# Kernel optimization log

Measured on AMD Instinct MI355X. Metric: run time of the kernel, lower is better.

## Reference

```python
import jax, jax.numpy as jnp
import numpy as np

B, C, H, W = 4, 256, 48, 48
NH = 4                 # num_heads
HD = C // NH           # head_dim = 64
KD = HD // 2           # key_dim = 32 (attn_ratio=0.5)
QKV_C = C + 2 * KD * NH  # 512
FF = 2 * C             # 512
EPS = 1e-3             # ultralytics BatchNorm2d eps


def _bn(x, g, b, m, v):
    # eval-mode BatchNorm2d over channel dim 1 of NCHW
    s = g / jnp.sqrt(v + EPS)
    return x * s[:, None, None] + (b - m * s)[:, None, None]


def _conv1x1(x, w):
    # w: [out_c, in_c]
    return jnp.einsum('bchw,oc->bohw', x, w)


def _dwconv3x3(x, w):
    # depthwise 3x3, padding 1; w: [C, 1, 3, 3]
    return jax.lax.conv_general_dilated(
        x, w, (1, 1), [(1, 1), (1, 1)],
        dimension_numbers=('NCHW', 'OIHW', 'NCHW'),
        feature_group_count=C)


def setup_inputs() -> dict:
    key = jax.random.key(0)
    ks = jax.random.split(key, 32)
    d = {}
    d['x'] = jax.random.normal(ks[0], (B, C, H, W), dtype=jnp.float32)

    def bn_params(i, ch):
        g = 0.5 + jax.random.uniform(ks[i], (ch,), dtype=jnp.float32)
        b = 0.1 * jax.random.normal(ks[i + 1], (ch,), dtype=jnp.float32)
        m = 0.1 * jax.random.normal(ks[i + 2], (ch,), dtype=jnp.float32)
        v = 0.5 + jax.random.uniform(ks[i + 3], (ch,), dtype=jnp.float32)
        return g, b, m, v

    d['qkv_w'] = 0.05 * jax.random.normal(ks[1], (QKV_C, C), dtype=jnp.float32)
    d['qkv_g'], d['qkv_b'], d['qkv_m'], d['qkv_v'] = bn_params(2, QKV_C)
    d['pe_w'] = 0.1 * jax.random.normal(ks[6], (C, 1, 3, 3), dtype=jnp.float32)
    d['pe_g'], d['pe_b'], d['pe_m'], d['pe_v'] = bn_params(7, C)
    d['proj_w'] = 0.05 * jax.random.normal(ks[11], (C, C), dtype=jnp.float32)
    d['proj_g'], d['proj_b'], d['proj_m'], d['proj_v'] = bn_params(12, C)
    d['f1_w'] = 0.05 * jax.random.normal(ks[16], (FF, C), dtype=jnp.float32)
    d['f1_g'], d['f1_b'], d['f1_m'], d['f1_v'] = bn_params(17, FF)
    d['f2_w'] = 0.05 * jax.random.normal(ks[21], (C, FF), dtype=jnp.float32)
    d['f2_g'], d['f2_b'], d['f2_m'], d['f2_v'] = bn_params(22, C)
    return d


def reference(x, qkv_w, qkv_g, qkv_b, qkv_m, qkv_v,
              pe_w, pe_g, pe_b, pe_m, pe_v,
              proj_w, proj_g, proj_b, proj_m, proj_v,
              f1_w, f1_g, f1_b, f1_m, f1_v,
              f2_w, f2_g, f2_b, f2_m, f2_v):
    b, c, h, w = x.shape
    n = h * w
    # --- Attention ---
    qkv = _bn(_conv1x1(x, qkv_w), qkv_g, qkv_b, qkv_m, qkv_v)
    qkv = qkv.reshape(b, NH, 2 * KD + HD, n)
    q = qkv[:, :, :KD]            # [b, nh, kd, n]
    k = qkv[:, :, KD:2 * KD]      # [b, nh, kd, n]
    v = qkv[:, :, 2 * KD:]        # [b, nh, hd, n]
    attn = jnp.einsum('bhkn,bhkm->bhnm', q, k) * (KD ** -0.5)
    attn = jax.nn.softmax(attn, axis=-1)
    o = jnp.einsum('bhdm,bhnm->bhdn', v, attn).reshape(b, c, h, w)
    pe = _bn(_dwconv3x3(v.reshape(b, c, h, w), pe_w), pe_g, pe_b, pe_m, pe_v)
    attn_out = _bn(_conv1x1(o + pe, proj_w), proj_g, proj_b, proj_m, proj_v)
    x = x + attn_out  # shortcut
    # --- FFN ---
    f = _conv1x1(x, f1_w)
    f = _bn(f, f1_g, f1_b, f1_m, f1_v)
    f = f * jax.nn.sigmoid(f)  # SiLU
    f = _bn(_conv1x1(f, f2_w), f2_g, f2_b, f2_m, f2_v)
    return x + f  # shortcut
```

## Files before the change

### kernel.cpp

```cpp
#include <hip/hip_runtime.h>
#include <math.h>

#define Bb   4
#define Cc   256
#define Hh   48
#define Ww   48
#define NNp  2304
#define Rr   9216
#define NHd  4
#define QKVC 512
#define EPSf 1e-3f

typedef unsigned int   u32;
typedef unsigned short u16;
typedef __attribute__((ext_vector_type(8))) __bf16 bf16x8;
typedef __attribute__((ext_vector_type(4))) float  f32x4;

#if __has_builtin(__builtin_amdgcn_exp2f)
#define EXP2F(x) __builtin_amdgcn_exp2f(x)
#else
#define EXP2F(x) __expf((x) * 0.6931471805599453f)
#endif

__device__ __forceinline__ u16 f2bf(float f) {
    u32 u = __float_as_uint(f);
    u = (u + 0x7fffu + ((u >> 16) & 1u)) >> 16;
    return (u16)u;
}
__device__ __forceinline__ float bf2f(u16 h) {
    return __uint_as_float((u32)h << 16);
}
__device__ __forceinline__ u32 pk2bf(float a, float b) {
    union { __bf16 h; u16 u; } ua, ub;
    ua.h = (__bf16)a; ub.h = (__bf16)b;
    return (u32)ua.u | ((u32)ub.u << 16);
}
__device__ __forceinline__ void gload16(const void* gsrc, void* ldst) {
    __builtin_amdgcn_global_load_lds(
        (const __attribute__((address_space(1))) u32*)gsrc,
        (__attribute__((address_space(3))) u32*)ldst, 16, 0, 0);
}

__global__ __launch_bounds__(64)
void prep_w(const float* __restrict__ W, const float* __restrict__ g,
            const float* __restrict__ b, const float* __restrict__ m,
            const float* __restrict__ v, u16* __restrict__ Wb,
            float* __restrict__ bias, int K, int qmode)
{
    const int oc = blockIdx.x;
    const int lane = threadIdx.x;
    const float s = g[oc] * rsqrtf(v[oc] + EPSf);
    const float c = (qmode == 1 && (oc & 127) < 32)
                  ? (0.17677669529663687f * 1.4426950408889634f) : 1.f;
    if (lane == 0) bias[oc] = (b[oc] - m[oc] * s) * c;
    const float sc = s * c;
    for (int k0 = lane * 4; k0 < K; k0 += 256) {
        const float4 w = *(const float4*)(W + (size_t)oc * K + k0);
        u32 lo = (u32)f2bf(w.x * sc) | ((u32)f2bf(w.y * sc) << 16);
        u32 hi = (u32)f2bf(w.z * sc) | ((u32)f2bf(w.w * sc) << 16);
        *(uint2*)(Wb + (size_t)oc * K + k0) = make_uint2(lo, hi);
    }
}

__global__ __launch_bounds__(256)
void cvt_x(const float* __restrict__ x, u16* __restrict__ Xt)
{
    const int b = blockIdx.z, c0 = blockIdx.y * 64, n0 = blockIdx.x * 64;
    __shared__ float tile[64][65];
    const int tid = threadIdx.x;
    {
        const int n = tid & 63, cl = tid >> 6;
        #pragma unroll
        for (int cc = 0; cc < 16; ++cc) {
            const int c = cc * 4 + cl;
            tile[c][n] = x[((size_t)b * Cc + c0 + c) * NNp + n0 + n];
        }
    }
    __syncthreads();
    {
        const int n = tid >> 2, q = tid & 3;
        #pragma unroll
        for (int j = 0; j < 2; ++j) {
            const int ch = q * 2 + j, c = ch * 8;
            u32 w[4];
            #pragma unroll
            for (int e = 0; e < 4; ++e)
                w[e] = (u32)f2bf(tile[c + 2*e][n]) | ((u32)f2bf(tile[c + 2*e + 1][n]) << 16);
            *(uint4*)(Xt + ((size_t)b * NNp + n0 + n) * Cc + c0 + c)
                = make_uint4(w[0], w[1], w[2], w[3]);
        }
    }
}

template<int BN_, int FN_, int MODE>
__global__ __launch_bounds__(256)
void gemm_mfma(const u16* __restrict__ A, const u16* __restrict__ Bx,
               const float* __restrict__ bias, const float* __restrict__ resid,
               float* __restrict__ Yf, u16* __restrict__ Yt, int M, int K)
{
    constexpr int WN = FN_ * 16;
    const int r0 = blockIdx.x * BN_;
    const int m0 = blockIdx.y * 128;
    const int tid = threadIdx.x;
    const int lane = tid & 63, wid = tid >> 6;
    const int g = lane >> 4, i16 = lane & 15;
    const int wr = wid >> 1, wc = wid & 1;

    __shared__ __align__(16) u16 Al[4][128][8];
    __shared__ __align__(16) u16 Bl[4][BN_][8];

    f32x4 acc[4][FN_];
    #pragma unroll
    for (int i = 0; i < 4; ++i)
        #pragma unroll
        for (int j = 0; j < FN_; ++j) acc[i][j] = (f32x4){0.f, 0.f, 0.f, 0.f};

    for (int k0 = 0; k0 < K; k0 += 32) {
        #pragma unroll
        for (int ii = 0; ii < 2; ++ii) {
            const int ci = ii * 256 + tid;
            gload16(A + (size_t)(m0 + (ci & 127)) * K + k0 + (ci >> 7) * 8,
                    &Al[0][0][0] + (size_t)ci * 8);
        }
        if (BN_ == 128) {
            #pragma unroll
            for (int ii = 0; ii < 2; ++ii) {
                const int ci = ii * 256 + tid;
                gload16(Bx + (size_t)(r0 + (ci & 127)) * K + k0 + (ci >> 7) * 8,
                        &Bl[0][0][0] + (size_t)ci * 8);
            }
        } else {
            gload16(Bx + (size_t)(r0 + (tid & 63)) * K + k0 + (tid >> 6) * 8,
                    &Bl[0][0][0] + (size_t)tid * 8);
        }
        __syncthreads();
        bf16x8 af[4], bf[FN_];
        #pragma unroll
        for (int ao = 0; ao < 4; ++ao)
            af[ao] = *(const bf16x8*)&Al[g][wr * 64 + ao * 16 + i16][0];
        #pragma unroll
        for (int bo = 0; bo < FN_; ++bo)
            bf[bo] = *(const bf16x8*)&Bl[g][wc * WN + bo * 16 + i16][0];
        #pragma unroll
        for (int ao = 0; ao < 4; ++ao)
            #pragma unroll
            for (int bo = 0; bo < FN_; ++bo)
                acc[ao][bo] = __builtin_amdgcn_mfma_f32_16x16x32_bf16(
                    af[ao], bf[bo], acc[ao][bo], 0, 0, 0);
        __syncthreads();
    }

    const int b  = r0 / NNp;
    const int nb = r0 - b * NNp;
    #pragma unroll
    for (int ao = 0; ao < 4; ++ao) {
        const int oc0 = m0 + wr * 64 + ao * 16 + g * 4;
        const float4 t4 = *(const float4*)(bias + oc0);
        #pragma unroll
        for (int bo = 0; bo < FN_; ++bo) {
            const int nloc = wc * WN + bo * 16 + i16;
            float y[4];
            y[0] = acc[ao][bo][0] + t4.x;  y[1] = acc[ao][bo][1] + t4.y;
            y[2] = acc[ao][bo][2] + t4.z;  y[3] = acc[ao][bo][3] + t4.w;
            if (MODE == 1 || MODE == 3) {
                const int n = nb + nloc;
                const size_t base = ((size_t)b * M + oc0) * NNp + n;
                #pragma unroll
                for (int r = 0; r < 4; ++r) {
                    y[r] += resid[base + (size_t)r * NNp];
                    Yf[base + (size_t)r * NNp] = y[r];
                }
            }
            if (MODE == 2) {
                #pragma unroll
                for (int r = 0; r < 4; ++r) y[r] = y[r] / (1.f + __expf(-y[r]));
            }
            if (MODE != 3) {
                const size_t rG = (size_t)(r0 + nloc);
                u32 lo = (u32)f2bf(y[0]) | ((u32)f2bf(y[1]) << 16);
                u32 hi = (u32)f2bf(y[2]) | ((u32)f2bf(y[3]) << 16);
                *(uint2*)(Yt + rG * M + oc0) = make_uint2(lo, hi);
            }
        }
    }
}

__global__ __launch_bounds__(256)
void repack_v(const u16* __restrict__ Yt, u16* __restrict__ Vb)
{
    const int m0 = blockIdx.x * 64;
    const int h = blockIdx.y, b = blockIdx.z;
    const int bh = b * NHd + h;
    __shared__ u16 vt[64][72];
    const int tid = threadIdx.x;
    #pragma unroll
    for (int ii = 0; ii < 2; ++ii) {
        const int mm = ii * 32 + (tid >> 3);
        const int ch = tid & 7;
        *(uint4*)&vt[mm][ch * 8] =
            *(const uint4*)(Yt + ((size_t)b * NNp + m0 + mm) * QKVC + h * 128 + 64 + ch * 8);
    }
    __syncthreads();
    const int d = tid >> 2, mq = tid & 3;
    #pragma unroll
    for (int j = 0; j < 2; ++j) {
        const int mc = mq * 2 + j;
        u32 w[4];
        #pragma unroll
        for (int e = 0; e < 4; ++e)
            w[e] = (u32)vt[mc * 8 + 2*e][d] | ((u32)vt[mc * 8 + 2*e + 1][d] << 16);
        *(uint4*)(Vb + ((size_t)bh * 64 + d) * NNp + m0 + mc * 8)
            = make_uint4(w[0], w[1], w[2], w[3]);
    }
}

__global__ __launch_bounds__(256)
void attn_mfma(const u16* __restrict__ Yt, const u16* __restrict__ Vb,
               u16* __restrict__ Ot)
{
    __shared__ __align__(16) u16 Klds[2][4][64][8];
    __shared__ __align__(16) u16 Vlds[2][64 * 64];
    __shared__ __align__(16) u32 Plds[4][16][36];

    const int tid  = threadIdx.x;
    const int wid  = tid >> 6;
    const int lane = tid & 63;
    const int g    = lane >> 4;
    const int i16  = lane & 15;

    const int h = blockIdx.y, b = blockIdx.z;
    const int bh = b * NHd + h;
    const size_t bG = (size_t)b * NNp;
    const u16* Vg = Vb + (size_t)bh * 64 * NNp;

    const int nq = blockIdx.x * 64 + wid * 16 + i16;
    const bf16x8 qfrag = *(const bf16x8*)(Yt + (bG + nq) * QKVC + h * 128 + g * 8);

    f32x4 zero = {0.f, 0.f, 0.f, 0.f};
    f32x4 oacc[4];
    #pragma unroll
    for (int d = 0; d < 4; ++d) oacc[d] = zero;
    float m_run = -1e30f, l_run = 0.f;

    gload16(Yt + (bG + (tid & 63)) * QKVC + h * 128 + 32 + (tid >> 6) * 8,
            &Klds[0][0][0][0] + (size_t)tid * 8);
    #pragma unroll
    for (int ii = 0; ii < 2; ++ii) {
        const int idx = ii * 256 + tid;
        const int d = idx >> 3, xx = idx & 7;
        const int c = xx ^ (d & 7);
        gload16(Vg + (size_t)d * NNp + c * 8, &Vlds[0][idx * 8]);
    }
    __syncthreads();

    int cur = 0;
    for (int t = 0; t < 36; ++t) {
        if (t < 35) {
            const int m0 = (t + 1) * 64;
            gload16(Yt + (bG + m0 + (tid & 63)) * QKVC + h * 128 + 32 + (tid >> 6) * 8,
                    &Klds[cur ^ 1][0][0][0] + (size_t)tid * 8);
            #pragma unroll
            for (int ii = 0; ii < 2; ++ii) {
                const int idx = ii * 256 + tid;
                const int d = idx >> 3, xx = idx & 7;
                const int c = xx ^ (d & 7);
                gload16(Vg + (size_t)d * NNp + m0 + c * 8, &Vlds[cur ^ 1][idx * 8]);
            }
        }

        f32x4 sac[4];
        __builtin_amdgcn_s_setprio(1);
        #pragma unroll
        for (int j = 0; j < 4; ++j) {
            const bf16x8 kf = *(const bf16x8*)&Klds[cur][g][16 * j + i16][0];
            sac[j] = __builtin_amdgcn_mfma_f32_16x16x32_bf16(kf, qfrag, zero, 0, 0, 0);
        }
        __builtin_amdgcn_s_setprio(0);

        float pm = sac[0][0];
        #pragma unroll
        for (int j = 0; j < 4; ++j)
            #pragma unroll
            for (int r = 0; r < 4; ++r) pm = fmaxf(pm, sac[j][r]);
        pm = fmaxf(pm, __shfl_xor(pm, 16));
        pm = fmaxf(pm, __shfl_xor(pm, 32));

        if (!__all(pm <= m_run + 8.f)) {
            const float mn = fmaxf(m_run, pm);
            const float fc = EXP2F(m_run - mn);
            m_run = mn;
            l_run *= fc;
            #pragma unroll
            for (int d = 0; d < 4; ++d) {
                oacc[d][0] *= fc; oacc[d][1] *= fc;
                oacc[d][2] *= fc; oacc[d][3] *= fc;
            }
        }

        float p[4][4];
        float psum = 0.f;
        #pragma unroll
        for (int j = 0; j < 4; ++j)
            #pragma unroll
            for (int r = 0; r < 4; ++r) {
                p[j][r] = EXP2F(sac[j][r] - m_run);
                psum += p[j][r];
            }
        psum += __shfl_xor(psum, 16);
        psum += __shfl_xor(psum, 32);
        l_run += psum;

        {
            u32* prow = &Plds[wid][i16][0];
            #pragma unroll
            for (int j = 0; j < 4; ++j) {
                const u32 w0 = pk2bf(p[j][0], p[j][1]);
                const u32 w1 = pk2bf(p[j][2], p[j][3]);
                *(uint2*)&prow[8 * j + 2 * g] = make_uint2(w0, w1);
            }
        }

        const int d7 = i16 & 7;
        __builtin_amdgcn_s_setprio(1);
        #pragma unroll
        for (int s = 0; s < 2; ++s) {
            const bf16x8 pf = *(const bf16x8*)&Plds[wid][i16][16 * s + 4 * g];
            const int vch = (4 * s + g) ^ d7;
            #pragma unroll
            for (int db = 0; db < 4; ++db) {
                const bf16x8 vf = *(const bf16x8*)&Vlds[cur][(db * 16 + i16) * 64 + vch * 8];
                oacc[db] = __builtin_amdgcn_mfma_f32_16x16x32_bf16(vf, pf, oacc[db], 0, 0, 0);
            }
        }
        __builtin_amdgcn_s_setprio(0);

        __syncthreads();
        cur ^= 1;
    }

    const float linv = 1.f / l_run;
    u16* ob = Ot + (bG + nq) * Cc + h * 64;
    #pragma unroll
    for (int db = 0; db < 4; ++db) {
        u32 lo = (u32)f2bf(oacc[db][0] * linv) | ((u32)f2bf(oacc[db][1] * linv) << 16);
        u32 hi = (u32)f2bf(oacc[db][2] * linv) | ((u32)f2bf(oacc[db][3] * linv) << 16);
        *(uint2*)(ob + db * 16 + g * 4) = make_uint2(lo, hi);
    }
}

__global__ __launch_bounds__(256)
void pe_bn(const u16* __restrict__ Yt, const float* __restrict__ pw,
           const float* __restrict__ gg, const float* __restrict__ bb,
           const float* __restrict__ mm, const float* __restrict__ vv,
           u16* __restrict__ Ot)
{
    const int tid = threadIdx.x;
    const int h = blockIdx.y, b = blockIdx.z;
    const int p = blockIdx.x * 32 + (tid >> 3);
    const int ch = tid & 7;
    const int c0 = h * 64 + ch * 8;
    const int yy = p / Ww, xx = p - yy * Ww;

    float acc[8];
    #pragma unroll
    for (int j = 0; j < 8; ++j) acc[j] = 0.f;

    #pragma unroll
    for (int dy = -1; dy <= 1; ++dy) {
        const int Y = yy + dy;
        if (Y < 0 || Y >= Hh) continue;
        #pragma unroll
        for (int dx = -1; dx <= 1; ++dx) {
            const int X = xx + dx;
            if (X < 0 || X >= Ww) continue;
            const uint4 raw = *(const uint4*)(Yt +
                ((size_t)b * NNp + Y * Ww + X) * QKVC + h * 128 + 64 + ch * 8);
            const u32* rw = (const u32*)&raw;
            #pragma unroll
            for (int j = 0; j < 8; ++j) {
                const u16 hv = (u16)(rw[j >> 1] >> (16 * (j & 1)));
                acc[j] += pw[(size_t)(c0 + j) * 9 + (dy + 1) * 3 + (dx + 1)] * bf2f(hv);
            }
        }
    }

    u16* dst = Ot + ((size_t)b * NNp + p) * Cc + c0;
    uint4 old = *(uint4*)dst;
    u32* ow = (u32*)&old;
    u32 res[4];
    #pragma unroll
    for (int e = 0; e < 4; ++e) {
        u16 r0, r1;
        {
            const int j = 2 * e;
            const float s = gg[c0 + j] * rsqrtf(vv[c0 + j] + EPSf);
            const float t = bb[c0 + j] - mm[c0 + j] * s;
            r0 = f2bf(bf2f((u16)(ow[e] & 0xffff)) + acc[j] * s + t);
        }
        {
            const int j = 2 * e + 1;
            const float s = gg[c0 + j] * rsqrtf(vv[c0 + j] + EPSf);
            const float t = bb[c0 + j] - mm[c0 + j] * s;
            r1 = f2bf(bf2f((u16)(ow[e] >> 16)) + acc[j] * s + t);
        }
        res[e] = (u32)r0 | ((u32)r1 << 16);
    }
    *(uint4*)dst = make_uint4(res[0], res[1], res[2], res[3]);
}

extern "C" void kernel_launch(void* const* d_in, const int* in_sizes, int n_in,
                              void* d_out, int out_size, void* d_ws, size_t ws_size,
                              hipStream_t stream)
{
    const float* x      = (const float*)d_in[0];
    const float* qkv_w  = (const float*)d_in[1];
    const float* qkv_g  = (const float*)d_in[2];
    const float* qkv_b  = (const float*)d_in[3];
    const float* qkv_m  = (const float*)d_in[4];
    const float* qkv_v  = (const float*)d_in[5];
    const float* pe_w   = (const float*)d_in[6];
    const float* pe_g   = (const float*)d_in[7];
    const float* pe_b   = (const float*)d_in[8];
    const float* pe_m   = (const float*)d_in[9];
    const float* pe_v   = (const float*)d_in[10];
    const float* proj_w = (const float*)d_in[11];
    const float* proj_g = (const float*)d_in[12];
    const float* proj_b = (const float*)d_in[13];
    const float* proj_m = (const float*)d_in[14];
    const float* proj_v = (const float*)d_in[15];
    const float* f1_w   = (const float*)d_in[16];
    const float* f1_g   = (const float*)d_in[17];
    const float* f1_b   = (const float*)d_in[18];
    const float* f1_m   = (const float*)d_in[19];
    const float* f1_v   = (const float*)d_in[20];
    const float* f2_w   = (const float*)d_in[21];
    const float* f2_g   = (const float*)d_in[22];
    const float* f2_b   = (const float*)d_in[23];
    const float* f2_m   = (const float*)d_in[24];
    const float* f2_v   = (const float*)d_in[25];

    char* wsb = (char*)d_ws;
    u16*   Yt   = (u16*)(wsb);
    u16*   Xt   = (u16*)(wsb + 9437184);
    u16*   Vb   = (u16*)(wsb + 14155776);
    u16*   Ot   = (u16*)(wsb + 18874368);
    float* x1f  = (float*)(wsb + 23592960);
    u16*   Wq   = (u16*)(wsb + 33030144);
    u16*   Wp   = (u16*)(wsb + 33292288);
    u16*   W1   = (u16*)(wsb + 33423360);
    u16*   W2   = (u16*)(wsb + 33685504);
    float* biq  = (float*)(wsb + 33947648);
    float* bip  = (float*)(wsb + 33949696);
    float* bi1  = (float*)(wsb + 33950720);
    float* bi2  = (float*)(wsb + 33952768);
    u16*   Ft   = Yt;
    u16*   X1t  = Xt;
    float* out  = (float*)d_out;

    prep_w<<<dim3(512), dim3(64), 0, stream>>>(qkv_w, qkv_g, qkv_b, qkv_m, qkv_v, Wq, biq, 256, 1);
    prep_w<<<dim3(256), dim3(64), 0, stream>>>(proj_w, proj_g, proj_b, proj_m, proj_v, Wp, bip, 256, 0);
    prep_w<<<dim3(512), dim3(64), 0, stream>>>(f1_w, f1_g, f1_b, f1_m, f1_v, W1, bi1, 256, 0);
    prep_w<<<dim3(256), dim3(64), 0, stream>>>(f2_w, f2_g, f2_b, f2_m, f2_v, W2, bi2, 512, 0);
    cvt_x<<<dim3(36, 4, 4), dim3(256), 0, stream>>>(x, Xt);

    gemm_mfma<128, 4, 0><<<dim3(72, 4), dim3(256), 0, stream>>>(
        Wq, Xt, biq, nullptr, nullptr, Yt, QKVC, 256);

    repack_v<<<dim3(36, 4, 4), dim3(256), 0, stream>>>(Yt, Vb);
    attn_mfma<<<dim3(36, 4, 4), dim3(256), 0, stream>>>(Yt, Vb, Ot);
    pe_bn<<<dim3(72, 4, 4), dim3(256), 0, stream>>>(Yt, pe_w, pe_g, pe_b, pe_m, pe_v, Ot);

    gemm_mfma<64, 2, 1><<<dim3(144, 2), dim3(256), 0, stream>>>(
        Wp, Ot, bip, x, x1f, X1t, Cc, 256);

    gemm_mfma<128, 4, 2><<<dim3(72, 4), dim3(256), 0, stream>>>(
        W1, X1t, bi1, nullptr, nullptr, Ft, QKVC, 256);

    gemm_mfma<64, 2, 3><<<dim3(144, 2), dim3(256), 0, stream>>>(
        W2, Ft, bi2, x1f, out, nullptr, Cc, 512);
}
```

Measured before the change: 163.4 us.

## Double-buffer GEMM loads, split attention keys across waves, merge weight prep

The GEMM kernel now double-buffers its LDS A/B tiles, prefetching the next K slice while the MFMAs run on the current one. It also raises wave priority around the MFMA block. The attention kernel now processes 128 keys per tile. Each wave handles two 16-query fragments on half of the key range, computes the softmax row sums with an MFMA against a ones vector, and the two key halves are merged through LDS at the end. The four weight-prep launches are merged into one kernel, cutting launch overhead. These changes aim to hide load latency and reuse K/V fragments, at the cost of more LDS and registers and an extra cross-wave reduction.

```diff
diff --git a/kernel.cpp b/kernel.cpp
--- a/kernel.cpp
+++ b/kernel.cpp
@@ -42,17 +42,30 @@
 }
 
 __global__ __launch_bounds__(64)
-void prep_w(const float* __restrict__ W, const float* __restrict__ g,
-            const float* __restrict__ b, const float* __restrict__ m,
-            const float* __restrict__ v, u16* __restrict__ Wb,
-            float* __restrict__ bias, int K, int qmode)
-{
-    const int oc = blockIdx.x;
+void prep_all(const float* __restrict__ W0, const float* __restrict__ g0, const float* __restrict__ b0, const float* __restrict__ m0, const float* __restrict__ v0, u16* __restrict__ Wb0, float* __restrict__ bi0,
+              const float* __restrict__ W1, const float* __restrict__ g1, const float* __restrict__ b1, const float* __restrict__ m1, const float* __restrict__ v1, u16* __restrict__ Wb1, float* __restrict__ bi1,
+              const float* __restrict__ W2, const float* __restrict__ g2, const float* __restrict__ b2, const float* __restrict__ m2, const float* __restrict__ v2, u16* __restrict__ Wb2, float* __restrict__ bi2,
+              const float* __restrict__ W3, const float* __restrict__ g3, const float* __restrict__ b3, const float* __restrict__ m3, const float* __restrict__ v3, u16* __restrict__ Wb3, float* __restrict__ bi3)
+{
+    const int bid = blockIdx.x;
+    const float *W, *gp, *bp, *mp, *vp;
+    u16* Wb; float* bias;
+    int K = 256, oc;
+    float c = 1.f;
+    if (bid < 512) {
+        oc = bid; W = W0; gp = g0; bp = b0; mp = m0; vp = v0; Wb = Wb0; bias = bi0;
+        if ((oc & 127) < 32) c = 0.17677669529663687f * 1.4426950408889634f;
+    } else if (bid < 768) {
+        oc = bid - 512; W = W1; gp = g1; bp = b1; mp = m1; vp = v1; Wb = Wb1; bias = bi1;
+    } else if (bid < 1280) {
+        oc = bid - 768; W = W2; gp = g2; bp = b2; mp = m2; vp = v2; Wb = Wb2; bias = bi2;
+    } else {
+        oc = bid - 1280; W = W3; gp = g3; bp = b3; mp = m3; vp = v3; Wb = Wb3; bias = bi3;
+        K = 512;
+    }
     const int lane = threadIdx.x;
-    const float s = g[oc] * rsqrtf(v[oc] + EPSf);
-    const float c = (qmode == 1 && (oc & 127) < 32)
-                  ? (0.17677669529663687f * 1.4426950408889634f) : 1.f;
-    if (lane == 0) bias[oc] = (b[oc] - m[oc] * s) * c;
+    const float s = gp[oc] * rsqrtf(vp[oc] + EPSf);
+    if (lane == 0) bias[oc] = (bp[oc] - mp[oc] * s) * c;
     const float sc = s * c;
     for (int k0 = lane * 4; k0 < K; k0 += 256) {
         const float4 w = *(const float4*)(W + (size_t)oc * K + k0);
@@ -106,8 +119,8 @@
     const int g = lane >> 4, i16 = lane & 15;
     const int wr = wid >> 1, wc = wid & 1;
 
-    __shared__ __align__(16) u16 Al[4][128][8];
-    __shared__ __align__(16) u16 Bl[4][BN_][8];
+    __shared__ __align__(16) u16 Al[2][4][128][8];
+    __shared__ __align__(16) u16 Bl[2][4][BN_][8];
 
     f32x4 acc[4][FN_];
     #pragma unroll
@@ -115,39 +128,64 @@
         #pragma unroll
         for (int j = 0; j < FN_; ++j) acc[i][j] = (f32x4){0.f, 0.f, 0.f, 0.f};
 
-    for (int k0 = 0; k0 < K; k0 += 32) {
+    #pragma unroll
+    for (int ii = 0; ii < 2; ++ii) {
+        const int ci = ii * 256 + tid;
+        gload16(A + (size_t)(m0 + (ci & 127)) * K + (ci >> 7) * 8,
+                (u16*)&Al[0][0][0][0] + (size_t)ci * 8);
+    }
+    if (BN_ == 128) {
         #pragma unroll
         for (int ii = 0; ii < 2; ++ii) {
             const int ci = ii * 256 + tid;
-            gload16(A + (size_t)(m0 + (ci & 127)) * K + k0 + (ci >> 7) * 8,
-                    &Al[0][0][0] + (size_t)ci * 8);
-        }
-        if (BN_ == 128) {
+            gload16(Bx + (size_t)(r0 + (ci & 127)) * K + (ci >> 7) * 8,
+                    (u16*)&Bl[0][0][0][0] + (size_t)ci * 8);
+        }
+    } else {
+        gload16(Bx + (size_t)(r0 + (tid & 63)) * K + (tid >> 6) * 8,
+                (u16*)&Bl[0][0][0][0] + (size_t)tid * 8);
+    }
+    __syncthreads();
+
+    int buf = 0;
+    for (int k0 = 0; k0 < K; k0 += 32) {
+        if (k0 + 32 < K) {
+            const int kn = k0 + 32;
             #pragma unroll
             for (int ii = 0; ii < 2; ++ii) {
                 const int ci = ii * 256 + tid;
-                gload16(Bx + (size_t)(r0 + (ci & 127)) * K + k0 + (ci >> 7) * 8,
-                        &Bl[0][0][0] + (size_t)ci * 8);
-            }
-        } else {
-            gload16(Bx + (size_t)(r0 + (tid & 63)) * K + k0 + (tid >> 6) * 8,
-                    &Bl[0][0][0] + (size_t)tid * 8);
-        }
-        __syncthreads();
+                gload16(A + (size_t)(m0 + (ci & 127)) * K + kn + (ci >> 7) * 8,
+                        (u16*)&Al[buf ^ 1][0][0][0] + (size_t)ci * 8);
+            }
+            if (BN_ == 128) {
+                #pragma unroll
+                for (int ii = 0; ii < 2; ++ii) {
+                    const int ci = ii * 256 + tid;
+                    gload16(Bx + (size_t)(r0 + (ci & 127)) * K + kn + (ci >> 7) * 8,
+                            (u16*)&Bl[buf ^ 1][0][0][0] + (size_t)ci * 8);
+                }
+            } else {
+                gload16(Bx + (size_t)(r0 + (tid & 63)) * K + kn + (tid >> 6) * 8,
+                        (u16*)&Bl[buf ^ 1][0][0][0] + (size_t)tid * 8);
+            }
+        }
         bf16x8 af[4], bf[FN_];
         #pragma unroll
         for (int ao = 0; ao < 4; ++ao)
-            af[ao] = *(const bf16x8*)&Al[g][wr * 64 + ao * 16 + i16][0];
+            af[ao] = *(const bf16x8*)&Al[buf][g][wr * 64 + ao * 16 + i16][0];
         #pragma unroll
         for (int bo = 0; bo < FN_; ++bo)
-            bf[bo] = *(const bf16x8*)&Bl[g][wc * WN + bo * 16 + i16][0];
+            bf[bo] = *(const bf16x8*)&Bl[buf][g][wc * WN + bo * 16 + i16][0];
+        __builtin_amdgcn_s_setprio(1);
         #pragma unroll
         for (int ao = 0; ao < 4; ++ao)
             #pragma unroll
             for (int bo = 0; bo < FN_; ++bo)
                 acc[ao][bo] = __builtin_amdgcn_mfma_f32_16x16x32_bf16(
                     af[ao], bf[bo], acc[ao][bo], 0, 0, 0);
+        __builtin_amdgcn_s_setprio(0);
         __syncthreads();
+        buf ^= 1;
     }
 
     const int b  = r0 / NNp;
@@ -218,118 +256,139 @@
 void attn_mfma(const u16* __restrict__ Yt, const u16* __restrict__ Vb,
                u16* __restrict__ Ot)
 {
-    __shared__ __align__(16) u16 Klds[2][4][64][8];
-    __shared__ __align__(16) u16 Vlds[2][64 * 64];
-    __shared__ __align__(16) u32 Plds[4][16][36];
+    __shared__ __align__(16) u16 Klds[2][4][128][8];
+    __shared__ __align__(16) u16 Vlds[2][64][16][8];
+    __shared__ __align__(16) u32 Plds[4][2][16][36];
 
     const int tid  = threadIdx.x;
     const int wid  = tid >> 6;
     const int lane = tid & 63;
     const int g    = lane >> 4;
     const int i16  = lane & 15;
+    const int ksl  = wid >> 1;
+    const int qh   = wid & 1;
 
     const int h = blockIdx.y, b = blockIdx.z;
     const int bh = b * NHd + h;
     const size_t bG = (size_t)b * NNp;
     const u16* Vg = Vb + (size_t)bh * 64 * NNp;
 
-    const int nq = blockIdx.x * 64 + wid * 16 + i16;
-    const bf16x8 qfrag = *(const bf16x8*)(Yt + (bG + nq) * QKVC + h * 128 + g * 8);
-
-    f32x4 zero = {0.f, 0.f, 0.f, 0.f};
-    f32x4 oacc[4];
-    #pragma unroll
-    for (int d = 0; d < 4; ++d) oacc[d] = zero;
-    float m_run = -1e30f, l_run = 0.f;
-
-    gload16(Yt + (bG + (tid & 63)) * QKVC + h * 128 + 32 + (tid >> 6) * 8,
-            &Klds[0][0][0][0] + (size_t)tid * 8);
+    const int nq0 = blockIdx.x * 64 + qh * 32 + i16;
+    bf16x8 qfrag[2];
+    qfrag[0] = *(const bf16x8*)(Yt + (bG + nq0) * QKVC + h * 128 + g * 8);
+    qfrag[1] = *(const bf16x8*)(Yt + (bG + nq0 + 16) * QKVC + h * 128 + g * 8);
+
+    bf16x8 ones;
+    { uint4 ov = make_uint4(0x3f803f80u, 0x3f803f80u, 0x3f803f80u, 0x3f803f80u);
+      ones = *(bf16x8*)&ov; }
+
+    const f32x4 zero = {0.f, 0.f, 0.f, 0.f};
+    f32x4 oacc[2][4];
+    f32x4 lacc[2];
+    #pragma unroll
+    for (int f = 0; f < 2; ++f) {
+        lacc[f] = zero;
+        #pragma unroll
+        for (int d = 0; d < 4; ++d) oacc[f][d] = zero;
+    }
+    float m_run[2] = {-1e30f, -1e30f};
+
     #pragma unroll
     for (int ii = 0; ii < 2; ++ii) {
+        const int ci = ii * 256 + tid;
+        gload16(Yt + (bG + (ci & 127)) * QKVC + h * 128 + 32 + (ci >> 7) * 8,
+                (u16*)&Klds[0][0][0][0] + (size_t)ci * 8);
+    }
+    #pragma unroll
+    for (int ii = 0; ii < 4; ++ii) {
         const int idx = ii * 256 + tid;
-        const int d = idx >> 3, xx = idx & 7;
-        const int c = xx ^ (d & 7);
-        gload16(Vg + (size_t)d * NNp + c * 8, &Vlds[0][idx * 8]);
+        const int d = idx >> 4, cp = idx & 15;
+        gload16(Vg + (size_t)d * NNp + (cp ^ (d & 7)) * 8,
+                (u16*)&Vlds[0][0][0][0] + (size_t)idx * 8);
     }
     __syncthreads();
 
     int cur = 0;
-    for (int t = 0; t < 36; ++t) {
-        if (t < 35) {
-            const int m0 = (t + 1) * 64;
-            gload16(Yt + (bG + m0 + (tid & 63)) * QKVC + h * 128 + 32 + (tid >> 6) * 8,
-                    &Klds[cur ^ 1][0][0][0] + (size_t)tid * 8);
+    for (int t = 0; t < 18; ++t) {
+        if (t < 17) {
+            const int m0 = (t + 1) * 128;
             #pragma unroll
             for (int ii = 0; ii < 2; ++ii) {
+                const int ci = ii * 256 + tid;
+                gload16(Yt + (bG + m0 + (ci & 127)) * QKVC + h * 128 + 32 + (ci >> 7) * 8,
+                        (u16*)&Klds[cur ^ 1][0][0][0] + (size_t)ci * 8);
+            }
+            #pragma unroll
+            for (int ii = 0; ii < 4; ++ii) {
                 const int idx = ii * 256 + tid;
-                const int d = idx >> 3, xx = idx & 7;
-                const int c = xx ^ (d & 7);
-                gload16(Vg + (size_t)d * NNp + m0 + c * 8, &Vlds[cur ^ 1][idx * 8]);
-            }
-        }
-
-        f32x4 sac[4];
+                const int d = idx >> 4, cp = idx & 15;
+                gload16(Vg + (size_t)d * NNp + m0 + (cp ^ (d & 7)) * 8,
+                        (u16*)&Vlds[cur ^ 1][0][0][0] + (size_t)idx * 8);
+            }
+        }
+
+        bf16x8 kf[4];
+        #pragma unroll
+        for (int j = 0; j < 4; ++j)
+            kf[j] = *(const bf16x8*)&Klds[cur][g][ksl * 64 + 16 * j + i16][0];
+
+        f32x4 sac[2][4];
         __builtin_amdgcn_s_setprio(1);
         #pragma unroll
-        for (int j = 0; j < 4; ++j) {
-            const bf16x8 kf = *(const bf16x8*)&Klds[cur][g][16 * j + i16][0];
-            sac[j] = __builtin_amdgcn_mfma_f32_16x16x32_bf16(kf, qfrag, zero, 0, 0, 0);
-        }
+        for (int f = 0; f < 2; ++f)
+            #pragma unroll
+            for (int j = 0; j < 4; ++j)
+                sac[f][j] = __builtin_amdgcn_mfma_f32_16x16x32_bf16(
+                    kf[j], qfrag[f], zero, 0, 0, 0);
         __builtin_amdgcn_s_setprio(0);
 
-        float pm = sac[0][0];
-        #pragma unroll
-        for (int j = 0; j < 4; ++j)
-            #pragma unroll
-            for (int r = 0; r < 4; ++r) pm = fmaxf(pm, sac[j][r]);
-        pm = fmaxf(pm, __shfl_xor(pm, 16));
-        pm = fmaxf(pm, __shfl_xor(pm, 32));
-
-        if (!__all(pm <= m_run + 8.f)) {
-            const float mn = fmaxf(m_run, pm);
-            const float fc = EXP2F(m_run - mn);
-            m_run = mn;
-            l_run *= fc;
-            #pragma unroll
-            for (int d = 0; d < 4; ++d) {
-                oacc[d][0] *= fc; oacc[d][1] *= fc;
-                oacc[d][2] *= fc; oacc[d][3] *= fc;
-            }
-        }
-
-        float p[4][4];
-        float psum = 0.f;
-        #pragma unroll
-        for (int j = 0; j < 4; ++j)
-            #pragma unroll
-            for (int r = 0; r < 4; ++r) {
-                p[j][r] = EXP2F(sac[j][r] - m_run);
-                psum += p[j][r];
-            }
-        psum += __shfl_xor(psum, 16);
-        psum += __shfl_xor(psum, 32);
-        l_run += psum;
-
-        {
-            u32* prow = &Plds[wid][i16][0];
+        #pragma unroll
+        for (int f = 0; f < 2; ++f) {
+            float pm = sac[f][0][0];
+            #pragma unroll
+            for (int j = 0; j < 4; ++j)
+                #pragma unroll
+                for (int r = 0; r < 4; ++r) pm = fmaxf(pm, sac[f][j][r]);
+            pm = fmaxf(pm, __shfl_xor(pm, 16));
+            pm = fmaxf(pm, __shfl_xor(pm, 32));
+
+            if (!__all(pm <= m_run[f] + 8.f)) {
+                const float mn = fmaxf(m_run[f], pm);
+                const float fc = EXP2F(m_run[f] - mn);
+                m_run[f] = mn;
+                lacc[f][0] *= fc; lacc[f][1] *= fc;
+                lacc[f][2] *= fc; lacc[f][3] *= fc;
+                #pragma unroll
+                for (int d = 0; d < 4; ++d) {
+                    oacc[f][d][0] *= fc; oacc[f][d][1] *= fc;
+                    oacc[f][d][2] *= fc; oacc[f][d][3] *= fc;
+                }
+            }
+
+            u32* prow = &Plds[wid][f][i16][0];
             #pragma unroll
             for (int j = 0; j < 4; ++j) {
-                const u32 w0 = pk2bf(p[j][0], p[j][1]);
-                const u32 w1 = pk2bf(p[j][2], p[j][3]);
-                *(uint2*)&prow[8 * j + 2 * g] = make_uint2(w0, w1);
-            }
-        }
-
-        const int d7 = i16 & 7;
+                const float p0 = EXP2F(sac[f][j][0] - m_run[f]);
+                const float p1 = EXP2F(sac[f][j][1] - m_run[f]);
+                const float p2 = EXP2F(sac[f][j][2] - m_run[f]);
+                const float p3 = EXP2F(sac[f][j][3] - m_run[f]);
+                *(uint2*)&prow[8 * j + 2 * g] = make_uint2(pk2bf(p0, p1), pk2bf(p2, p3));
+            }
+        }
+
         __builtin_amdgcn_s_setprio(1);
         #pragma unroll
         for (int s = 0; s < 2; ++s) {
-            const bf16x8 pf = *(const bf16x8*)&Plds[wid][i16][16 * s + 4 * g];
-            const int vch = (4 * s + g) ^ d7;
+            const bf16x8 pf0 = *(const bf16x8*)&Plds[wid][0][i16][16 * s + 4 * g];
+            const bf16x8 pf1 = *(const bf16x8*)&Plds[wid][1][i16][16 * s + 4 * g];
+            lacc[0] = __builtin_amdgcn_mfma_f32_16x16x32_bf16(ones, pf0, lacc[0], 0, 0, 0);
+            lacc[1] = __builtin_amdgcn_mfma_f32_16x16x32_bf16(ones, pf1, lacc[1], 0, 0, 0);
+            const int cv = ksl * 8 + 4 * s + g;
             #pragma unroll
             for (int db = 0; db < 4; ++db) {
-                const bf16x8 vf = *(const bf16x8*)&Vlds[cur][(db * 16 + i16) * 64 + vch * 8];
-                oacc[db] = __builtin_amdgcn_mfma_f32_16x16x32_bf16(vf, pf, oacc[db], 0, 0, 0);
+                const bf16x8 vf = *(const bf16x8*)&Vlds[cur][db * 16 + i16][cv ^ (i16 & 7)][0];
+                oacc[0][db] = __builtin_amdgcn_mfma_f32_16x16x32_bf16(vf, pf0, oacc[0][db], 0, 0, 0);
+                oacc[1][db] = __builtin_amdgcn_mfma_f32_16x16x32_bf16(vf, pf1, oacc[1][db], 0, 0, 0);
             }
         }
         __builtin_amdgcn_s_setprio(0);
@@ -338,13 +397,41 @@
         cur ^= 1;
     }
 
-    const float linv = 1.f / l_run;
-    u16* ob = Ot + (bG + nq) * Cc + h * 64;
-    #pragma unroll
-    for (int db = 0; db < 4; ++db) {
-        u32 lo = (u32)f2bf(oacc[db][0] * linv) | ((u32)f2bf(oacc[db][1] * linv) << 16);
-        u32 hi = (u32)f2bf(oacc[db][2] * linv) | ((u32)f2bf(oacc[db][3] * linv) << 16);
-        *(uint2*)(ob + db * 16 + g * 4) = make_uint2(lo, hi);
+    float* Ml = (float*)&Vlds[0][0][0][0];
+    if (wid >= 2) {
+        #pragma unroll
+        for (int f = 0; f < 2; ++f) {
+            float* dst = Ml + ((size_t)((qh * 2 + f) * 64 + lane)) * 20;
+            dst[0] = m_run[f];
+            dst[1] = lacc[f][0];
+            #pragma unroll
+            for (int db = 0; db < 4; ++db)
+                #pragma unroll
+                for (int e = 0; e < 4; ++e)
+                    dst[2 + db * 4 + e] = oacc[f][db][e];
+        }
+    }
+    __syncthreads();
+    if (wid < 2) {
+        #pragma unroll
+        for (int f = 0; f < 2; ++f) {
+            const float* src = Ml + ((size_t)((qh * 2 + f) * 64 + lane)) * 20;
+            const float m2 = src[0], l2 = src[1];
+            const float mn = fmaxf(m_run[f], m2);
+            const float fa = EXP2F(m_run[f] - mn);
+            const float fb = EXP2F(m2 - mn);
+            const float linv = 1.f / (lacc[f][0] * fa + l2 * fb);
+            u16* ob = Ot + (bG + nq0 + f * 16) * Cc + h * 64;
+            #pragma unroll
+            for (int db = 0; db < 4; ++db) {
+                const float y0 = (oacc[f][db][0] * fa + src[2 + db * 4 + 0] * fb) * linv;
+                const float y1 = (oacc[f][db][1] * fa + src[2 + db * 4 + 1] * fb) * linv;
+                const float y2 = (oacc[f][db][2] * fa + src[2 + db * 4 + 2] * fb) * linv;
+                const float y3 = (oacc[f][db][3] * fa + src[2 + db * 4 + 3] * fb) * linv;
+                *(uint2*)(ob + db * 16 + g * 4) =
+                    make_uint2(pk2bf(y0, y1), pk2bf(y2, y3));
+            }
+        }
     }
 }
 
@@ -457,10 +544,11 @@
     u16*   X1t  = Xt;
     float* out  = (float*)d_out;
 
-    prep_w<<<dim3(512), dim3(64), 0, stream>>>(qkv_w, qkv_g, qkv_b, qkv_m, qkv_v, Wq, biq, 256, 1);
-    prep_w<<<dim3(256), dim3(64), 0, stream>>>(proj_w, proj_g, proj_b, proj_m, proj_v, Wp, bip, 256, 0);
-    prep_w<<<dim3(512), dim3(64), 0, stream>>>(f1_w, f1_g, f1_b, f1_m, f1_v, W1, bi1, 256, 0);
-    prep_w<<<dim3(256), dim3(64), 0, stream>>>(f2_w, f2_g, f2_b, f2_m, f2_v, W2, bi2, 512, 0);
+    prep_all<<<dim3(1536), dim3(64), 0, stream>>>(
+        qkv_w, qkv_g, qkv_b, qkv_m, qkv_v, Wq, biq,
+        proj_w, proj_g, proj_b, proj_m, proj_v, Wp, bip,
+        f1_w, f1_g, f1_b, f1_m, f1_v, W1, bi1,
+        f2_w, f2_g, f2_b, f2_m, f2_v, W2, bi2);
     cvt_x<<<dim3(36, 4, 4), dim3(256), 0, stream>>>(x, Xt);
 
     gemm_mfma<128, 4, 0><<<dim3(72, 4), dim3(256), 0, stream>>>(
```

Result: slower. 166.9 us (+2.1%).
